# Kernel optimization log

Hardware: AMD Instinct MI355X
Metric: run time of the kernel (lower is better)

Reference implementation:

```python
import jax, jax.numpy as jnp
import numpy as np

HIDDEN = 1024
NUM_HEADS = 16
HEAD_DIM = HIDDEN // NUM_HEADS


def setup_inputs() -> dict:
    key = jax.random.key(0)
    k1, k2, k3, k4, k5 = jax.random.split(key, 5)
    B, S, T, H = 2, 2048, 2048, HIDDEN
    scale = 0.02
    return {
        "query": jax.random.normal(k1, (B, S, H), dtype=jnp.float32),
        "key_value": jax.random.normal(k2, (B, T, H), dtype=jnp.float32),
        "Wq": jax.random.normal(k3, (H, H), dtype=jnp.float32) * scale,
        "Wkv": jax.random.normal(k4, (H, 2 * H), dtype=jnp.float32) * scale,
        "Wc": jax.random.normal(k5, (H, H), dtype=jnp.float32) * scale,
    }


def reference(query, key_value, Wq, Wkv, Wc):
    B, S, H = query.shape
    T = key_value.shape[1]
    nh, hd = NUM_HEADS, HEAD_DIM

    q = query @ Wq                                  # [B,S,H]
    kv = key_value @ Wkv                            # [B,T,2H]
    k, v = kv[..., :H], kv[..., H:]

    # [B, nh, S|T, hd]
    q = q.reshape(B, S, nh, hd).transpose(0, 2, 1, 3)
    k = k.reshape(B, T, nh, hd).transpose(0, 2, 1, 3)
    v = v.reshape(B, T, nh, hd).transpose(0, 2, 1, 3)

    scale = hd ** -0.5
    scores = jnp.einsum("bhsd,bhtd->bhst", q * scale, k)   # [B,nh,S,T]
    probs = jax.nn.softmax(scores, axis=-1)
    y = jnp.einsum("bhst,bhtd->bhsd", probs, v)             # [B,nh,S,hd]
    y = y.transpose(0, 2, 1, 3).reshape(B, S, H)
    return y @ Wc
```

## Files before the change

kernel.cpp:

```cpp
#include <hip/hip_runtime.h>
#include <hip/hip_bf16.h>


typedef unsigned short u16;
typedef __attribute__((ext_vector_type(4))) float float4v;
typedef __attribute__((ext_vector_type(4))) unsigned short u16x4;
typedef __attribute__((ext_vector_type(8))) short short8;
typedef __attribute__((ext_vector_type(4))) float floatx4;

__device__ __forceinline__ u16 f2bf(float f) {
  unsigned u = __float_as_uint(f);
  u += 0x7fffu + ((u >> 16) & 1u);
  return (u16)(u >> 16);
}

__device__ __forceinline__ float fast_exp2(float x) {
#if __has_builtin(__builtin_amdgcn_exp2f)
  return __builtin_amdgcn_exp2f(x);
#else
  return exp2f(x);
#endif
}

__device__ __forceinline__ unsigned pack_bf2(float a, float b) {
#if __has_builtin(__builtin_amdgcn_cvt_pk_bf16_f32)
  auto r = __builtin_amdgcn_cvt_pk_bf16_f32(a, b);
  unsigned u;
  __builtin_memcpy(&u, &r, 4);
  return u;
#else
  unsigned ua = __float_as_uint(a) + 0x8000u;
  unsigned ub = __float_as_uint(b) + 0x8000u;
  return __builtin_amdgcn_perm(ub, ua, 0x07060302u);
#endif
}

__device__ __forceinline__ void store_out(float* p, float v) { *p = v; }
__device__ __forceinline__ void store_out(u16* p, float v) { *p = f2bf(v); }

__device__ __forceinline__ void gld16(const void* g, void* l) {
  __builtin_amdgcn_global_load_lds(
      (const __attribute__((address_space(1))) void*)g,
      (__attribute__((address_space(3))) void*)l, 16, 0, 0);
}

__global__ void cvt_bf16_2(const float* __restrict__ a, const float* __restrict__ b,
                           u16* __restrict__ oa, u16* __restrict__ ob, int n4) {
  int i = blockIdx.x * blockDim.x + threadIdx.x;
  if (i >= n4) return;
  const float* src = blockIdx.y ? b : a;
  u16* dst = blockIdx.y ? ob : oa;
  float4v v = ((const float4v*)src)[i];
  u16x4 o;
  o.x = f2bf(v.x); o.y = f2bf(v.y); o.z = f2bf(v.z); o.w = f2bf(v.w);
  ((u16x4*)dst)[i] = o;
}

__global__ void transpose_cvt3(const float* __restrict__ Wq,
                               const float* __restrict__ Wkv,
                               const float* __restrict__ Wc,
                               u16* __restrict__ Wqt, u16* __restrict__ Wkvt,
                               u16* __restrict__ Wct) {
  __shared__ float tile[32][33];
  const int z = blockIdx.z;
  const float* in = z == 0 ? Wq : (z == 1 ? Wkv : Wc);
  u16* out = z == 0 ? Wqt : (z == 1 ? Wkvt : Wct);
  const int C = (z == 1) ? 2048 : 1024;
  const int R = 1024;
  int bx = blockIdx.x * 32;
  if (bx >= C) return;
  int by = blockIdx.y * 32;
  int tx = threadIdx.x, ty = threadIdx.y;
#pragma unroll
  for (int i = 0; i < 32; i += 8)
    tile[ty + i][tx] = in[(size_t)(by + ty + i) * C + bx + tx];
  __syncthreads();
#pragma unroll
  for (int i = 0; i < 32; i += 8)
    out[(size_t)(bx + ty + i) * R + by + tx] = f2bf(tile[tx][ty + i]);
}

template <typename OutT, int NI>
__device__ __forceinline__ void gemm_body(const u16* __restrict__ A,
                                          const u16* __restrict__ Bt,
                                          OutT* __restrict__ C,
                                          int N, int lda, int Klen, float scale,
                                          int bm, int bn,
                                          u16* As, u16* Bs) {
  const int t = threadIdx.x;
  const int w = t >> 6, l = t & 63;
  const int lane15 = l & 15, quad = l >> 4;
  const int wm = w >> 1, wn = w & 1;
  const int x3 = lane15 & 3;
  const int BSZ = NI * 1024;

  const int srow = t >> 2;
  const int scol = (((t & 3) ^ (srow & 3)) << 3);
  const u16* ag0 = A + (size_t)(bm + srow) * lda + scol;
  const u16* ag1 = ag0 + (size_t)64 * lda;
  const u16* bg0 = Bt + (size_t)(bn + srow) * lda + scol;
  const u16* bg1 = bg0 + (size_t)64 * lda;

  int afo[4], bfo[NI];
#pragma unroll
  for (int mi = 0; mi < 4; ++mi)
    afo[mi] = (wm * 64 + mi * 16 + lane15) * 32 + ((quad ^ x3) << 3);
#pragma unroll
  for (int ni = 0; ni < NI; ++ni)
    bfo[ni] = (wn * (NI * 16) + ni * 16 + lane15) * 32 + ((quad ^ x3) << 3);

  floatx4 acc[4][NI] = {};

  auto stage = [&](int kt, int ab, int bb) {
    gld16(ag0 + kt, &As[ab + t * 8]);
    gld16(ag1 + kt, &As[ab + 2048 + t * 8]);
    gld16(bg0 + kt, &Bs[bb + t * 8]);
    if (NI == 4) gld16(bg1 + kt, &Bs[bb + 2048 + t * 8]);
  };
  auto compute = [&](int ab, int bb) {
    short8 af[4], bf[NI];
#pragma unroll
    for (int mi = 0; mi < 4; ++mi) af[mi] = *(const short8*)&As[ab + afo[mi]];
#pragma unroll
    for (int ni = 0; ni < NI; ++ni) bf[ni] = *(const short8*)&Bs[bb + bfo[ni]];
#pragma unroll
    for (int mi = 0; mi < 4; ++mi)
#pragma unroll
      for (int ni = 0; ni < NI; ++ni)
        acc[mi][ni] = __builtin_amdgcn_mfma_f32_16x16x32_bf16(af[mi], bf[ni],
                                                              acc[mi][ni], 0, 0, 0);
  };

  stage(0, 0, 0);
  __syncthreads();
  for (int kt = 0; kt < Klen; kt += 64) {
    if (kt + 32 < Klen) stage(kt + 32, 4096, BSZ);
    compute(0, 0);
    __syncthreads();
    if (kt + 64 < Klen) stage(kt + 64, 0, 0);
    compute(4096, BSZ);
    __syncthreads();
  }

#pragma unroll
  for (int mi = 0; mi < 4; ++mi)
#pragma unroll
    for (int ni = 0; ni < NI; ++ni) {
      int col = bn + wn * (NI * 16) + ni * 16 + lane15;
#pragma unroll
      for (int r = 0; r < 4; ++r) {
        int row = bm + wm * 64 + mi * 16 + quad * 4 + r;
        store_out(&C[(size_t)row * N + col], acc[mi][ni][r] * scale);
      }
    }
}

__global__ __launch_bounds__(256) void gemm_qkv(const u16* __restrict__ qin,
                                                const u16* __restrict__ kvin,
                                                const u16* __restrict__ Wqt,
                                                const u16* __restrict__ Wkvt,
                                                u16* __restrict__ qp,
                                                u16* __restrict__ kvp,
                                                float qscale) {
  __shared__ __align__(16) u16 As[2 * 4096];
  __shared__ __align__(16) u16 Bs[2 * 4096];
  const bool isq = blockIdx.x < 8;
  const u16* A = isq ? qin : kvin;
  const u16* Bt = isq ? Wqt : Wkvt;
  u16* C = isq ? qp : kvp;
  const int N = isq ? 1024 : 2048;
  const int bn = (isq ? blockIdx.x : blockIdx.x - 8) * 128;
  const float scale = isq ? qscale : 1.0f;
  gemm_body<u16, 4>(A, Bt, C, N, 1024, 1024, scale, blockIdx.y * 128, bn, As, Bs);
}

__global__ __launch_bounds__(256) void gemm_out(const u16* __restrict__ A,
                                                const u16* __restrict__ Bt,
                                                float* __restrict__ P0,
                                                float* __restrict__ P1) {
  __shared__ __align__(16) u16 As[2 * 4096];
  __shared__ __align__(16) u16 Bs[2 * 4096];
  const int k0 = blockIdx.z * 512;
  float* dst = blockIdx.z ? P1 : P0;
  gemm_body<float, 4>(A + k0, Bt + k0, dst, 1024, 1024, 512, 1.0f,
                      blockIdx.y * 128, blockIdx.x * 128, As, Bs);
}

__global__ void add_f32(float* __restrict__ out, const float* __restrict__ p1, int n4) {
  int i = blockIdx.x * blockDim.x + threadIdx.x;
  if (i >= n4) return;
  float4v a = ((const float4v*)out)[i];
  float4v b = ((const float4v*)p1)[i];
  a.x += b.x; a.y += b.y; a.z += b.z; a.w += b.w;
  ((float4v*)out)[i] = a;
}

__global__ __launch_bounds__(256) void transpose_v(const u16* __restrict__ KV,
                                                   u16* __restrict__ VT) {
  __shared__ __align__(16) u16 tile[64 * 72];
  const int bh = blockIdx.y, b = bh >> 4, h = bh & 15;
  const int t0 = blockIdx.x * 64;
  const int t = threadIdx.x;
#pragma unroll
  for (int c = t; c < 512; c += 256) {
    int row = c >> 3, col8 = (c & 7) << 3;
    *(short8*)&tile[row * 72 + col8] =
        *(const short8*)&KV[(size_t)(b * 2048 + t0 + row) * 2048 + 1024 + h * 64 + col8];
  }
  __syncthreads();
#pragma unroll
  for (int c = t; c < 512; c += 256) {
    int d = c >> 3, t8 = (c & 7) << 3;
    short8 v;
#pragma unroll
    for (int j = 0; j < 8; ++j) v[j] = (short)tile[(t8 + j) * 72 + d];
    *(short8*)&VT[(size_t)(bh * 64 + d) * 2048 + t0 + t8] = v;
  }
}

__global__ __launch_bounds__(512) void attn_kern(const u16* __restrict__ Q,
                                                 const u16* __restrict__ KV,
                                                 const u16* __restrict__ VT,
                                                 u16* __restrict__ Y) {
  __shared__ __align__(16) u16 Ks[2 * 4096];
  __shared__ __align__(16) u16 VTs[2 * 4096];
  __shared__ __align__(16) u16 Ps[8192];
  const int t = threadIdx.x, w = t >> 6, l = t & 63;
  const int lane15 = l & 15, quad = l >> 4;
  const int bh = blockIdx.y, b = bh >> 4, h = bh & 15;
  const int qrow0 = b * 2048 + blockIdx.x * 128;
  const int xm = lane15 & 7;

  short8 qf[2];
#pragma unroll
  for (int ks = 0; ks < 2; ++ks)
    qf[ks] = *(const short8*)&Q[(size_t)(qrow0 + w * 16 + lane15) * 1024 +
                                h * 64 + ks * 32 + quad * 8];

  const short8 vones = {0x3F80, 0x3F80, 0x3F80, 0x3F80,
                        0x3F80, 0x3F80, 0x3F80, 0x3F80};

  floatx4 yacc[4] = {};
  floatx4 lacc = {};

  const int srow = t >> 3;
  const int scol = (((t & 7) ^ (srow & 7)) << 3);
  const u16* kg = KV + (size_t)(b * 2048 + srow) * 2048 + h * 64 + scol;
  const u16* vg = VT + (size_t)(bh * 64 + srow) * 2048 + scol;

  const int prow = (w * 16 + lane15) * 64;
  int kfo[2][4], vfo[2][4], pwo[4], pro[2];
#pragma unroll
  for (int ks = 0; ks < 2; ++ks)
#pragma unroll
    for (int ti = 0; ti < 4; ++ti)
      kfo[ks][ti] = (ti * 16 + lane15) * 64 + (((ks * 4 + quad) ^ xm) << 3);
#pragma unroll
  for (int ts = 0; ts < 2; ++ts) {
#pragma unroll
    for (int ni = 0; ni < 4; ++ni)
      vfo[ts][ni] = (ni * 16 + lane15) * 64 + (((ts * 4 + quad) ^ xm) << 3);
    pro[ts] = prow + (((ts * 4 + quad) ^ xm) << 3);
  }
#pragma unroll
  for (int ti = 0; ti < 4; ++ti)
    pwo[ti] = prow + (((ti * 2 + (quad >> 1)) ^ xm) << 3) + ((quad & 1) << 2);

  auto stage = [&](int t0n, int buf) {
    gld16(kg + (size_t)t0n * 2048, &Ks[buf + t * 8]);
    gld16(vg + t0n, &VTs[buf + t * 8]);
  };
  auto compute = [&](int buf) {
    floatx4 sacc[4] = {};
#pragma unroll
    for (int ks = 0; ks < 2; ++ks)
#pragma unroll
      for (int ti = 0; ti < 4; ++ti) {
        short8 kf = *(const short8*)&Ks[buf + kfo[ks][ti]];
        sacc[ti] = __builtin_amdgcn_mfma_f32_16x16x32_bf16(kf, qf[ks], sacc[ti], 0, 0, 0);
      }
#pragma unroll
    for (int ti = 0; ti < 4; ++ti) {
      float p0 = fast_exp2(sacc[ti][0]);
      float p1 = fast_exp2(sacc[ti][1]);
      float p2 = fast_exp2(sacc[ti][2]);
      float p3 = fast_exp2(sacc[ti][3]);
      uint2 pk;
      pk.x = pack_bf2(p0, p1);
      pk.y = pack_bf2(p2, p3);
      *(uint2*)&Ps[pwo[ti]] = pk;
    }
#pragma unroll
    for (int ts = 0; ts < 2; ++ts) {
      short8 pf = *(const short8*)&Ps[pro[ts]];
      lacc = __builtin_amdgcn_mfma_f32_16x16x32_bf16(pf, vones, lacc, 0, 0, 0);
#pragma unroll
      for (int ni = 0; ni < 4; ++ni) {
        short8 vf = *(const short8*)&VTs[buf + vfo[ts][ni]];
        yacc[ni] = __builtin_amdgcn_mfma_f32_16x16x32_bf16(pf, vf, yacc[ni], 0, 0, 0);
      }
    }
  };

  stage(0, 0);
  __syncthreads();
  for (int t0 = 0; t0 < 2048; t0 += 128) {
    if (t0 + 64 < 2048) stage(t0 + 64, 4096);
    compute(0);
    __syncthreads();
    if (t0 + 128 < 2048) stage(t0 + 128, 0);
    compute(4096);
    __syncthreads();
  }

#pragma unroll
  for (int r = 0; r < 4; ++r) {
    float linv = 1.0f / lacc[r];
    int row = qrow0 + w * 16 + quad * 4 + r;
#pragma unroll
    for (int ni = 0; ni < 4; ++ni)
      Y[(size_t)row * 1024 + h * 64 + ni * 16 + lane15] = f2bf(yacc[ni][r] * linv);
  }
}

extern "C" void kernel_launch(void* const* d_in, const int* in_sizes, int n_in,
                              void* d_out, int out_size, void* d_ws, size_t ws_size,
                              hipStream_t stream) {
  const float* query = (const float*)d_in[0];
  const float* key_value = (const float*)d_in[1];
  const float* Wq = (const float*)d_in[2];
  const float* Wkv = (const float*)d_in[3];
  const float* Wc = (const float*)d_in[4];
  float* out = (float*)d_out;

  const size_t MB = 1024 * 1024;
  char* ws = (char*)d_ws;
  u16* qin  = (u16*)(ws + 0 * MB);
  u16* kvin = (u16*)(ws + 8 * MB);
  u16* Wqt  = (u16*)(ws + 16 * MB);
  u16* Wkvt = (u16*)(ws + 18 * MB);
  u16* Wct  = (u16*)(ws + 22 * MB);
  u16* qp   = (u16*)(ws + 24 * MB);
  u16* kvp  = (u16*)(ws + 32 * MB);
  u16* vt   = (u16*)(ws + 48 * MB);
  u16* y    = (u16*)(ws + 56 * MB);
  float* p1 = (float*)(ws + 0 * MB);

  const int nAct4 = 2 * 2048 * 1024 / 4;
  cvt_bf16_2<<<dim3(nAct4 / 256, 2), dim3(256), 0, stream>>>(query, key_value,
                                                             qin, kvin, nAct4);
  transpose_cvt3<<<dim3(64, 32, 3), dim3(32, 8), 0, stream>>>(Wq, Wkv, Wc,
                                                              Wqt, Wkvt, Wct);

  const float qscale = 0.125f * 1.4426950408889634f;
  gemm_qkv<<<dim3(24, 32), dim3(256), 0, stream>>>(qin, kvin, Wqt, Wkvt, qp, kvp, qscale);
  transpose_v<<<dim3(32, 32), dim3(256), 0, stream>>>(kvp, vt);
  attn_kern<<<dim3(16, 32), dim3(512), 0, stream>>>(qp, kvp, vt, y);
  gemm_out<<<dim3(8, 32, 2), dim3(256), 0, stream>>>(y, Wct, out, p1);
  add_f32<<<dim3(nAct4 / 256), dim3(256), 0, stream>>>(out, p1, nAct4);
}
```

Before: 211.8 us.

## Fuse activation conversion and V transpose into QKV GEMM; drop split-K output GEMM

The QKV projection now reads fp32 activations straight into LDS and converts them to bf16 while building MFMA fragments, so the separate conversion kernel goes away. V tiles are computed with swapped MFMA operands and written already transposed, which removes the transpose_v kernel, and K gets its own compact buffer. The output projection drops split-K plus the add kernel in favour of a single full-K GEMM with 64-wide N tiles. The cost is twice the LDS traffic for fp32 A tiles, conversion work repeated in the inner loop, and strided stores for V^T.

```diff
diff --git a/kernel.cpp b/kernel.cpp
--- a/kernel.cpp
+++ b/kernel.cpp
@@ -4,7 +4,6 @@
 
 typedef unsigned short u16;
 typedef __attribute__((ext_vector_type(4))) float float4v;
-typedef __attribute__((ext_vector_type(4))) unsigned short u16x4;
 typedef __attribute__((ext_vector_type(8))) short short8;
 typedef __attribute__((ext_vector_type(4))) float floatx4;
 
@@ -29,8 +28,8 @@
   __builtin_memcpy(&u, &r, 4);
   return u;
 #else
-  unsigned ua = __float_as_uint(a) + 0x8000u;
-  unsigned ub = __float_as_uint(b) + 0x8000u;
+  unsigned ua = __float_as_uint(a) + 0x7fffu + ((__float_as_uint(a) >> 16) & 1u);
+  unsigned ub = __float_as_uint(b) + 0x7fffu + ((__float_as_uint(b) >> 16) & 1u);
   return __builtin_amdgcn_perm(ub, ua, 0x07060302u);
 #endif
 }
@@ -42,18 +41,6 @@
   __builtin_amdgcn_global_load_lds(
       (const __attribute__((address_space(1))) void*)g,
       (__attribute__((address_space(3))) void*)l, 16, 0, 0);
-}
-
-__global__ void cvt_bf16_2(const float* __restrict__ a, const float* __restrict__ b,
-                           u16* __restrict__ oa, u16* __restrict__ ob, int n4) {
-  int i = blockIdx.x * blockDim.x + threadIdx.x;
-  if (i >= n4) return;
-  const float* src = blockIdx.y ? b : a;
-  u16* dst = blockIdx.y ? ob : oa;
-  float4v v = ((const float4v*)src)[i];
-  u16x4 o;
-  o.x = f2bf(v.x); o.y = f2bf(v.y); o.z = f2bf(v.z); o.w = f2bf(v.w);
-  ((u16x4*)dst)[i] = o;
 }
 
 __global__ void transpose_cvt3(const float* __restrict__ Wq,
@@ -80,6 +67,148 @@
     out[(size_t)(bx + ty + i) * R + by + tx] = f2bf(tile[tx][ty + i]);
 }
 
+__global__ __launch_bounds__(256) void gemm_qkv(const float* __restrict__ X,
+                                                const float* __restrict__ KV,
+                                                const u16* __restrict__ Wqt,
+                                                const u16* __restrict__ Wkvt,
+                                                u16* __restrict__ qp,
+                                                u16* __restrict__ kp,
+                                                u16* __restrict__ vt,
+                                                float qscale) {
+  __shared__ __align__(16) float Asf[2 * 4096];
+  __shared__ __align__(16) u16 Bs[2 * 4096];
+  const int t = threadIdx.x;
+  const int w = t >> 6, l = t & 63;
+  const int lane15 = l & 15, quad = l >> 4;
+  const int wm = w >> 1, wn = w & 1;
+  const int x3 = lane15 & 3, x7 = lane15 & 7;
+  const int bm = blockIdx.y * 128;
+
+  const int bx = blockIdx.x;
+  const int mode = bx >> 3;
+  const float* A = (mode == 0) ? X : KV;
+  const u16* Bt = (mode == 0) ? Wqt : Wkvt;
+  const int bnw = (mode == 2) ? 1024 + (bx - 16) * 128 : (bx & 7) * 128;
+
+  const int arow = t >> 3;
+  const int acc_ = ((t & 7) ^ ((t >> 3) & 7)) << 2;
+  const float* ag[4];
+#pragma unroll
+  for (int j = 0; j < 4; ++j)
+    ag[j] = A + (size_t)(bm + arow + j * 32) * 1024 + acc_;
+  const int brow = t >> 2;
+  const int bcc = ((t & 3) ^ ((t >> 2) & 3)) << 3;
+  const u16* bg[2];
+#pragma unroll
+  for (int j = 0; j < 2; ++j)
+    bg[j] = Bt + (size_t)(bnw + brow + j * 64) * 1024 + bcc;
+
+  int afo0[4], afo1[4], bfo[4];
+#pragma unroll
+  for (int mi = 0; mi < 4; ++mi) {
+    int row = wm * 64 + mi * 16 + lane15;
+    afo0[mi] = row * 32 + (((quad * 2) ^ x7) << 2);
+    afo1[mi] = row * 32 + (((quad * 2 + 1) ^ x7) << 2);
+  }
+#pragma unroll
+  for (int ni = 0; ni < 4; ++ni)
+    bfo[ni] = (wn * 64 + ni * 16 + lane15) * 32 + ((quad ^ x3) << 3);
+
+  floatx4 acc[4][4] = {};
+  const bool vswap = (mode == 2);
+
+  auto stage = [&](int kt, int buf) {
+#pragma unroll
+    for (int j = 0; j < 4; ++j)
+      gld16(ag[j] + kt, &Asf[buf * 4096 + (t + j * 256) * 4]);
+#pragma unroll
+    for (int j = 0; j < 2; ++j)
+      gld16(bg[j] + kt, &Bs[buf * 4096 + (t + j * 256) * 8]);
+  };
+  auto compute = [&](int buf) {
+    short8 af[4], bf[4];
+#pragma unroll
+    for (int mi = 0; mi < 4; ++mi) {
+      float4v f0 = *(const float4v*)&Asf[buf * 4096 + afo0[mi]];
+      float4v f1 = *(const float4v*)&Asf[buf * 4096 + afo1[mi]];
+      union { short8 s; unsigned u[4]; } tmp;
+      tmp.u[0] = pack_bf2(f0.x, f0.y);
+      tmp.u[1] = pack_bf2(f0.z, f0.w);
+      tmp.u[2] = pack_bf2(f1.x, f1.y);
+      tmp.u[3] = pack_bf2(f1.z, f1.w);
+      af[mi] = tmp.s;
+    }
+#pragma unroll
+    for (int ni = 0; ni < 4; ++ni) bf[ni] = *(const short8*)&Bs[buf * 4096 + bfo[ni]];
+    if (!vswap) {
+#pragma unroll
+      for (int mi = 0; mi < 4; ++mi)
+#pragma unroll
+        for (int ni = 0; ni < 4; ++ni)
+          acc[mi][ni] = __builtin_amdgcn_mfma_f32_16x16x32_bf16(af[mi], bf[ni],
+                                                                acc[mi][ni], 0, 0, 0);
+    } else {
+#pragma unroll
+      for (int mi = 0; mi < 4; ++mi)
+#pragma unroll
+        for (int ni = 0; ni < 4; ++ni)
+          acc[mi][ni] = __builtin_amdgcn_mfma_f32_16x16x32_bf16(bf[ni], af[mi],
+                                                                acc[mi][ni], 0, 0, 0);
+    }
+  };
+
+  stage(0, 0);
+  __syncthreads();
+  for (int kt = 0; kt < 1024; kt += 64) {
+    if (kt + 32 < 1024) stage(kt + 32, 1);
+    compute(0);
+    __syncthreads();
+    if (kt + 64 < 1024) stage(kt + 64, 0);
+    compute(1);
+    __syncthreads();
+  }
+
+  if (mode == 0) {
+#pragma unroll
+    for (int mi = 0; mi < 4; ++mi)
+#pragma unroll
+      for (int ni = 0; ni < 4; ++ni) {
+        int col = bnw + wn * 64 + ni * 16 + lane15;
+#pragma unroll
+        for (int r = 0; r < 4; ++r) {
+          int row = bm + wm * 64 + mi * 16 + quad * 4 + r;
+          qp[(size_t)row * 1024 + col] = f2bf(acc[mi][ni][r] * qscale);
+        }
+      }
+  } else if (mode == 1) {
+#pragma unroll
+    for (int mi = 0; mi < 4; ++mi)
+#pragma unroll
+      for (int ni = 0; ni < 4; ++ni) {
+        int col = bnw + wn * 64 + ni * 16 + lane15;
+#pragma unroll
+        for (int r = 0; r < 4; ++r) {
+          int row = bm + wm * 64 + mi * 16 + quad * 4 + r;
+          kp[(size_t)row * 1024 + col] = f2bf(acc[mi][ni][r]);
+        }
+      }
+  } else {
+    const int b = bm >> 11;
+    const int tbase = (bm & 2047) + wm * 64;
+#pragma unroll
+    for (int mi = 0; mi < 4; ++mi)
+#pragma unroll
+      for (int ni = 0; ni < 4; ++ni) {
+        int tloc = tbase + mi * 16 + lane15;
+#pragma unroll
+        for (int r = 0; r < 4; ++r) {
+          int wc = (bnw - 1024) + wn * 64 + ni * 16 + quad * 4 + r;
+          vt[(size_t)(b * 1024 + wc) * 2048 + tloc] = f2bf(acc[mi][ni][r]);
+        }
+      }
+  }
+}
+
 template <typename OutT, int NI>
 __device__ __forceinline__ void gemm_body(const u16* __restrict__ A,
                                           const u16* __restrict__ Bt,
@@ -155,71 +284,17 @@
     }
 }
 
-__global__ __launch_bounds__(256) void gemm_qkv(const u16* __restrict__ qin,
-                                                const u16* __restrict__ kvin,
-                                                const u16* __restrict__ Wqt,
-                                                const u16* __restrict__ Wkvt,
-                                                u16* __restrict__ qp,
-                                                u16* __restrict__ kvp,
-                                                float qscale) {
-  __shared__ __align__(16) u16 As[2 * 4096];
-  __shared__ __align__(16) u16 Bs[2 * 4096];
-  const bool isq = blockIdx.x < 8;
-  const u16* A = isq ? qin : kvin;
-  const u16* Bt = isq ? Wqt : Wkvt;
-  u16* C = isq ? qp : kvp;
-  const int N = isq ? 1024 : 2048;
-  const int bn = (isq ? blockIdx.x : blockIdx.x - 8) * 128;
-  const float scale = isq ? qscale : 1.0f;
-  gemm_body<u16, 4>(A, Bt, C, N, 1024, 1024, scale, blockIdx.y * 128, bn, As, Bs);
-}
-
 __global__ __launch_bounds__(256) void gemm_out(const u16* __restrict__ A,
                                                 const u16* __restrict__ Bt,
-                                                float* __restrict__ P0,
-                                                float* __restrict__ P1) {
+                                                float* __restrict__ C) {
   __shared__ __align__(16) u16 As[2 * 4096];
-  __shared__ __align__(16) u16 Bs[2 * 4096];
-  const int k0 = blockIdx.z * 512;
-  float* dst = blockIdx.z ? P1 : P0;
-  gemm_body<float, 4>(A + k0, Bt + k0, dst, 1024, 1024, 512, 1.0f,
-                      blockIdx.y * 128, blockIdx.x * 128, As, Bs);
-}
-
-__global__ void add_f32(float* __restrict__ out, const float* __restrict__ p1, int n4) {
-  int i = blockIdx.x * blockDim.x + threadIdx.x;
-  if (i >= n4) return;
-  float4v a = ((const float4v*)out)[i];
-  float4v b = ((const float4v*)p1)[i];
-  a.x += b.x; a.y += b.y; a.z += b.z; a.w += b.w;
-  ((float4v*)out)[i] = a;
-}
-
-__global__ __launch_bounds__(256) void transpose_v(const u16* __restrict__ KV,
-                                                   u16* __restrict__ VT) {
-  __shared__ __align__(16) u16 tile[64 * 72];
-  const int bh = blockIdx.y, b = bh >> 4, h = bh & 15;
-  const int t0 = blockIdx.x * 64;
-  const int t = threadIdx.x;
-#pragma unroll
-  for (int c = t; c < 512; c += 256) {
-    int row = c >> 3, col8 = (c & 7) << 3;
-    *(short8*)&tile[row * 72 + col8] =
-        *(const short8*)&KV[(size_t)(b * 2048 + t0 + row) * 2048 + 1024 + h * 64 + col8];
-  }
-  __syncthreads();
-#pragma unroll
-  for (int c = t; c < 512; c += 256) {
-    int d = c >> 3, t8 = (c & 7) << 3;
-    short8 v;
-#pragma unroll
-    for (int j = 0; j < 8; ++j) v[j] = (short)tile[(t8 + j) * 72 + d];
-    *(short8*)&VT[(size_t)(bh * 64 + d) * 2048 + t0 + t8] = v;
-  }
+  __shared__ __align__(16) u16 Bs[2 * 2048];
+  gemm_body<float, 2>(A, Bt, C, 1024, 1024, 1024, 1.0f, blockIdx.y * 128,
+                      blockIdx.x * 64, As, Bs);
 }
 
 __global__ __launch_bounds__(512) void attn_kern(const u16* __restrict__ Q,
-                                                 const u16* __restrict__ KV,
+                                                 const u16* __restrict__ KP,
                                                  const u16* __restrict__ VT,
                                                  u16* __restrict__ Y) {
   __shared__ __align__(16) u16 Ks[2 * 4096];
@@ -245,7 +320,7 @@
 
   const int srow = t >> 3;
   const int scol = (((t & 7) ^ (srow & 7)) << 3);
-  const u16* kg = KV + (size_t)(b * 2048 + srow) * 2048 + h * 64 + scol;
+  const u16* kg = KP + (size_t)(b * 2048 + srow) * 1024 + h * 64 + scol;
   const u16* vg = VT + (size_t)(bh * 64 + srow) * 2048 + scol;
 
   const int prow = (w * 16 + lane15) * 64;
@@ -267,7 +342,7 @@
     pwo[ti] = prow + (((ti * 2 + (quad >> 1)) ^ xm) << 3) + ((quad & 1) << 2);
 
   auto stage = [&](int t0n, int buf) {
-    gld16(kg + (size_t)t0n * 2048, &Ks[buf + t * 8]);
+    gld16(kg + (size_t)t0n * 1024, &Ks[buf + t * 8]);
     gld16(vg + t0n, &VTs[buf + t * 8]);
   };
   auto compute = [&](int buf) {
@@ -335,27 +410,19 @@
 
   const size_t MB = 1024 * 1024;
   char* ws = (char*)d_ws;
-  u16* qin  = (u16*)(ws + 0 * MB);
-  u16* kvin = (u16*)(ws + 8 * MB);
-  u16* Wqt  = (u16*)(ws + 16 * MB);
-  u16* Wkvt = (u16*)(ws + 18 * MB);
-  u16* Wct  = (u16*)(ws + 22 * MB);
-  u16* qp   = (u16*)(ws + 24 * MB);
-  u16* kvp  = (u16*)(ws + 32 * MB);
-  u16* vt   = (u16*)(ws + 48 * MB);
-  u16* y    = (u16*)(ws + 56 * MB);
-  float* p1 = (float*)(ws + 0 * MB);
-
-  const int nAct4 = 2 * 2048 * 1024 / 4;
-  cvt_bf16_2<<<dim3(nAct4 / 256, 2), dim3(256), 0, stream>>>(query, key_value,
-                                                             qin, kvin, nAct4);
+  u16* Wqt  = (u16*)(ws + 0 * MB);
+  u16* Wkvt = (u16*)(ws + 2 * MB);
+  u16* Wct  = (u16*)(ws + 6 * MB);
+  u16* qp   = (u16*)(ws + 8 * MB);
+  u16* kp   = (u16*)(ws + 16 * MB);
+  u16* vt   = (u16*)(ws + 24 * MB);
+  u16* y    = (u16*)(ws + 32 * MB);
+
   transpose_cvt3<<<dim3(64, 32, 3), dim3(32, 8), 0, stream>>>(Wq, Wkv, Wc,
                                                               Wqt, Wkvt, Wct);
-
   const float qscale = 0.125f * 1.4426950408889634f;
-  gemm_qkv<<<dim3(24, 32), dim3(256), 0, stream>>>(qin, kvin, Wqt, Wkvt, qp, kvp, qscale);
-  transpose_v<<<dim3(32, 32), dim3(256), 0, stream>>>(kvp, vt);
-  attn_kern<<<dim3(16, 32), dim3(512), 0, stream>>>(qp, kvp, vt, y);
-  gemm_out<<<dim3(8, 32, 2), dim3(256), 0, stream>>>(y, Wct, out, p1);
-  add_f32<<<dim3(nAct4 / 256), dim3(256), 0, stream>>>(out, p1, nAct4);
-}
+  gemm_qkv<<<dim3(24, 32), dim3(256), 0, stream>>>(query, key_value, Wqt, Wkvt,
+                                                   qp, kp, vt, qscale);
+  attn_kern<<<dim3(16, 32), dim3(512), 0, stream>>>(qp, kp, vt, y);
+  gemm_out<<<dim3(16, 32), dim3(256), 0, stream>>>(y, Wct, out);
+}
```

Result: slower. 261.9 us (+23.6%).
